# Performance work log

Hardware: AMD Instinct MI355X
Metric: run time of the kernel (lower is better)

## Reference

```python
import jax, jax.numpy as jnp
import numpy as np

# dims
D_IN, D, H, HD = 1536, 256, 8, 32
DEPTH, FFN = 2, 1024
B, L = 1, 8191
NGRIDS, TILE = 256, 256
SEGMENTS = [1024, 2048, 4096, 8192, 16384]   # get_optimal_segment_length(32768, 256)
RATIOS = [1, 2, 4, 8, 16]                    # LongNet canonical dilation ratios
SCALE = HD ** -0.5


def setup_inputs() -> dict:
    key = jax.random.key(0)
    ks = jax.random.split(key, 16)
    w = lambda k, s: jax.random.normal(k, s, jnp.float32) * 0.02
    return {
        "x": jax.random.normal(ks[0], (B, L, D_IN), jnp.float32),
        "coords": jax.random.randint(ks[1], (B, L, 2), 0, NGRIDS * TILE, jnp.int32),
        "proj_w": w(ks[2], (D_IN, D)), "proj_b": jnp.zeros((D,), jnp.float32),
        "cls_tok": w(ks[3], (1, 1, D)),
        "Wq": w(ks[4], (DEPTH, D, D)), "Wk": w(ks[5], (DEPTH, D, D)),
        "Wv": w(ks[6], (DEPTH, D, D)), "Wo": w(ks[7], (DEPTH, D, D)),
        "bq": jnp.zeros((DEPTH, D), jnp.float32), "bk": jnp.zeros((DEPTH, D), jnp.float32),
        "bv": jnp.zeros((DEPTH, D), jnp.float32), "bo": jnp.zeros((DEPTH, D), jnp.float32),
        "ln1_g": jnp.ones((DEPTH, D), jnp.float32), "ln1_b": jnp.zeros((DEPTH, D), jnp.float32),
        "ln2_g": jnp.ones((DEPTH, D), jnp.float32), "ln2_b": jnp.zeros((DEPTH, D), jnp.float32),
        "W1": w(ks[8], (DEPTH, D, FFN)), "b1": jnp.zeros((DEPTH, FFN), jnp.float32),
        "W2": w(ks[9], (DEPTH, FFN, D)), "b2": jnp.zeros((DEPTH, D), jnp.float32),
        "enc_g": jnp.ones((D,), jnp.float32), "enc_b": jnp.zeros((D,), jnp.float32),
        "norm_g": jnp.ones((D,), jnp.float32), "norm_b": jnp.zeros((D,), jnp.float32),
    }


def _ln(x, g, b):
    mu = x.mean(-1, keepdims=True)
    v = ((x - mu) ** 2).mean(-1, keepdims=True)
    return (x - mu) * jax.lax.rsqrt(v + 1e-5) * g + b


def _pos_table():
    # MAE-style 2D sincos pos embed, row 0 = cls (zeros). [NGRIDS^2+1, D]
    g = jnp.arange(NGRIDS, dtype=jnp.float32)
    gw, gh = jnp.meshgrid(g, g)  # gw[i,j]=j, gh[i,j]=i; flatten index = i*NGRIDS + j
    def one(pos):
        omega = 1.0 / (10000.0 ** (jnp.arange(D // 4, dtype=jnp.float32) / (D // 4)))
        o = pos.reshape(-1)[:, None] * omega[None]
        return jnp.concatenate([jnp.sin(o), jnp.cos(o)], -1)
    tab = jnp.concatenate([one(gw), one(gh)], -1)
    return jnp.concatenate([jnp.zeros((1, D), jnp.float32), tab], 0)


def _dilated_attn(q, k, v):
    # q,k,v: [B,S,H,HD]. LongNet: per (segment w, dilation r) branch, sparse in-segment
    # attention on stride-r rows (head-dependent offset h%r), branches fused via their
    # softmax log-sum-exp weights.
    S = q.shape[1]
    hh = jnp.arange(H)[:, None]
    outs, lses = [], []
    for w, r in zip(SEGMENTS, RATIOS):
        n = (S + w - 1) // w
        Sp = n * w
        def seg(t):
            tp = jnp.pad(t, ((0, 0), (0, Sp - S), (0, 0), (0, 0)))
            return tp.reshape(B, n, w, H, HD).transpose(0, 1, 3, 2, 4)  # [B,n,H,w,HD]
        qs_, ks_, vs_ = seg(q), seg(k), seg(v)
        t = w // r
        idx = (hh % r) + r * jnp.arange(t)[None, :]                  # [H,t]
        qs = qs_[:, :, hh, idx]                                      # [B,n,H,t,HD]
        ks = ks_[:, :, hh, idx]
        vs = vs_[:, :, hh, idx]
        valid = (jnp.arange(n)[:, None, None] * w + idx[None]) < S   # [n,H,t]
        sc = jnp.einsum('bnhtd,bnhsd->bnhts', qs, ks) * SCALE
        sc = jnp.where(valid[None, :, :, None, :], sc, -1e9)
        m = sc.max(-1, keepdims=True)
        p = jnp.exp(sc - m)
        den = p.sum(-1, keepdims=True)
        o = jnp.einsum('bnhts,bnhsd->bnhtd', p, vs) / den
        lse = m[..., 0] + jnp.log(den[..., 0])                       # [B,n,H,t]
        fo = jnp.zeros((B, n, H, w, HD), q.dtype).at[:, :, hh, idx].set(o)
        fl = jnp.full((B, n, H, w), -1e30, q.dtype).at[:, :, hh, idx].set(lse)
        outs.append(fo.transpose(0, 1, 3, 2, 4).reshape(B, Sp, H, HD)[:, :S])
        lses.append(fl.transpose(0, 1, 3, 2).reshape(B, Sp, H)[:, :S])
    Ls = jnp.stack(lses)   # [5,B,S,H]
    Os = jnp.stack(outs)   # [5,B,S,H,HD]
    wts = jnp.exp(Ls - Ls.max(0, keepdims=True))
    return (wts[..., None] * Os).sum(0) / wts.sum(0)[..., None]


def _forward(x, coords, proj_w, proj_b, cls_tok, Wq, Wk, Wv, Wo, bq, bk, bv, bo,
             ln1_g, ln1_b, ln2_g, ln2_b, W1, b1, W2, b2, enc_g, enc_b, norm_g, norm_b):
    h = x @ proj_w + proj_b                                   # patch embed [B,L,D]
    tab = _pos_table()
    cg = jnp.floor(coords.astype(jnp.float32) / TILE).astype(jnp.int32)
    pos = cg[..., 0] * NGRIDS + cg[..., 1] + 1                # coords_to_pos
    h = h + tab[pos]
    cls = jnp.broadcast_to(cls_tok + tab[0], (B, 1, D))
    h = jnp.concatenate([cls, h], 1)                          # [B,S,D], S = L+1
    S = h.shape[1]
    for i in range(DEPTH):                                    # pre-LN LongNet encoder layers
        a = _ln(h, ln1_g[i], ln1_b[i])
        q = (a @ Wq[i] + bq[i]).reshape(B, S, H, HD)
        k = (a @ Wk[i] + bk[i]).reshape(B, S, H, HD)
        v = (a @ Wv[i] + bv[i]).reshape(B, S, H, HD)
        o = _dilated_attn(q, k, v).reshape(B, S, D)
        h = h + o @ Wo[i] + bo[i]
        f = _ln(h, ln2_g[i], ln2_b[i])
        h = h + jax.nn.gelu(f @ W1[i] + b1[i], approximate=False) @ W2[i] + b2[i]
    h = _ln(h, enc_g, enc_b)     # encoder final LN
    h = _ln(h, norm_g, norm_b)   # model self.norm
    return h[:, 0]               # cls embedding (global_pool=False)


def reference(x, coords, proj_w, proj_b, cls_tok, Wq, Wk, Wv, Wo, bq, bk, bv, bo,
              ln1_g, ln1_b, ln2_g, ln2_b, W1, b1, W2, b2, enc_g, enc_b, norm_g, norm_b):
    return _forward(x, coords, proj_w, proj_b, cls_tok, Wq, Wk, Wv, Wo, bq, bk, bv, bo,
                    ln1_g, ln1_b, ln2_g, ln2_b, W1, b1, W2, b2, enc_g, enc_b, norm_g, norm_b)
```

## Files before the change

### kernel.cpp

```cpp
#include <hip/hip_runtime.h>
#include <math.h>

#define S_TOT 8192
#define DD 256
#define NHEAD 8
#define HDSZ 32
#define ATT_SCALE 0.17677669529663687f
#define ATT_SCALE_LOG2E 0.25506601f

typedef short short8 __attribute__((ext_vector_type(8)));
typedef float f32x4 __attribute__((ext_vector_type(4)));
typedef unsigned short ushort;

#define OFF_PROJ 0
#define OFF_WQ0  393216
#define OFF_WK0  458752
#define OFF_WV0  524288
#define OFF_WO0  589824
#define OFF_W10  655360
#define OFF_W20  917504
#define OFF_WK1  1179648
#define OFF_WV1  1245184
#define OFF_WQ1  1310720
#define OFF_WO1  1376256
#define OFF_W11  1441792
#define OFF_W21  1703936
#define WBUF_TOT 1966080

__device__ inline ushort f2bf(float f) {
    union { float f; unsigned u; } c; c.f = f;
    unsigned u = c.u;
    u += 0x7fffu + ((u >> 16) & 1u);
    return (ushort)(u >> 16);
}
__device__ inline float bf2f(ushort u) {
    union { unsigned u; float f; } c; c.u = ((unsigned)u) << 16;
    return c.f;
}
__device__ inline float gelu_exact(float v) {
    return 0.5f * v * (1.0f + erff(v * 0.7071067811865475f));
}
__device__ inline float block_sum256(float v, float* red) {
    #pragma unroll
    for (int off = 32; off > 0; off >>= 1) v += __shfl_down(v, off, 64);
    const int wid = threadIdx.x >> 6, lane = threadIdx.x & 63;
    if (lane == 0) red[wid] = v;
    __syncthreads();
    const float s = red[0] + red[1] + red[2] + red[3];
    __syncthreads();
    return s;
}

__global__ __launch_bounds__(256)
void setup_kernel(const float* __restrict__ x, const float* __restrict__ proj_w,
                  const float* __restrict__ Wq, const float* __restrict__ Wk,
                  const float* __restrict__ Wv, const float* __restrict__ Wo,
                  const float* __restrict__ W1, const float* __restrict__ W2,
                  const float* __restrict__ bq, const float* __restrict__ bk,
                  const float* __restrict__ bv, const float* __restrict__ cls_tok,
                  ushort* __restrict__ wbuf, float* __restrict__ bqkv0,
                  float* __restrict__ bkv1, ushort* __restrict__ xbf,
                  float* __restrict__ h)
{
    const int b = blockIdx.x;
    const int t = threadIdx.x;
    if (b >= 482) {
        if (b == 6626) { h[t] = cls_tok[t]; return; }
        const int i = (b - 482) * 256 + t;
        const int n8 = 8191 * 1536 / 8;
        if (i >= n8) return;
        const float4 a0 = *(const float4*)(x + (size_t)i * 8);
        const float4 a1 = *(const float4*)(x + (size_t)i * 8 + 4);
        ushort tmp[8] = { f2bf(a0.x), f2bf(a0.y), f2bf(a0.z), f2bf(a0.w),
                          f2bf(a1.x), f2bf(a1.y), f2bf(a1.z), f2bf(a1.w) };
        *(uint4*)(xbf + (size_t)i * 8) = *(const uint4*)tmp;
        return;
    }
    if (b >= 480) {
        if (b == 480) {
            for (int i = t; i < 768; i += 256)
                bqkv0[i] = (i < 256) ? bq[i] : ((i < 512) ? bk[i - 256] : bv[i - 512]);
        } else {
            for (int i = t; i < 512; i += 256)
                bkv1[i] = (i < 256) ? bk[256 + i] : bv[i];
        }
        return;
    }
    const float* src; ushort* dst; int R, C, t0;
    if (b < 96)       { src = proj_w;        dst = wbuf + OFF_PROJ; R = 1536; C = 256;  t0 = 0;   }
    else if (b < 112) { src = Wq;            dst = wbuf + OFF_WQ0;  R = 256;  C = 256;  t0 = 96;  }
    else if (b < 128) { src = Wk;            dst = wbuf + OFF_WK0;  R = 256;  C = 256;  t0 = 112; }
    else if (b < 144) { src = Wv;            dst = wbuf + OFF_WV0;  R = 256;  C = 256;  t0 = 128; }
    else if (b < 160) { src = Wo;            dst = wbuf + OFF_WO0;  R = 256;  C = 256;  t0 = 144; }
    else if (b < 224) { src = W1;            dst = wbuf + OFF_W10;  R = 256;  C = 1024; t0 = 160; }
    else if (b < 288) { src = W2;            dst = wbuf + OFF_W20;  R = 1024; C = 256;  t0 = 224; }
    else if (b < 304) { src = Wk + 65536;    dst = wbuf + OFF_WK1;  R = 256;  C = 256;  t0 = 288; }
    else if (b < 320) { src = Wv + 65536;    dst = wbuf + OFF_WV1;  R = 256;  C = 256;  t0 = 304; }
    else if (b < 336) { src = Wq + 65536;    dst = wbuf + OFF_WQ1;  R = 256;  C = 256;  t0 = 320; }
    else if (b < 352) { src = Wo + 65536;    dst = wbuf + OFF_WO1;  R = 256;  C = 256;  t0 = 336; }
    else if (b < 416) { src = W1 + 262144;   dst = wbuf + OFF_W11;  R = 256;  C = 1024; t0 = 352; }
    else              { src = W2 + 262144;   dst = wbuf + OFF_W21;  R = 1024; C = 256;  t0 = 416; }
    const int lt = b - t0;
    const int tC = C >> 6;
    const int tr = lt / tC, tc = lt % tC;
    __shared__ ushort tile[64][68];
    const int col = t & 63;
    const int r4  = t >> 6;
    #pragma unroll
    for (int i = 0; i < 16; ++i) {
        const int row = i * 4 + r4;
        tile[row][col] = f2bf(src[(size_t)(tr * 64 + row) * C + tc * 64 + col]);
    }
    __syncthreads();
    #pragma unroll
    for (int i = 0; i < 16; ++i) {
        const int n = i * 4 + r4;
        dst[(size_t)(tc * 64 + n) * R + tr * 64 + col] = tile[col][n];
    }
}

__global__ __launch_bounds__(256)
void ln_kernel(const float* __restrict__ in, const float* __restrict__ g,
               const float* __restrict__ b, ushort* __restrict__ outp)
{
    __shared__ float red[4];
    const int row = blockIdx.x;
    const int d = threadIdx.x;
    const float xv = in[(size_t)row * DD + d];
    const float mu = block_sum256(xv, red) * (1.0f / 256.0f);
    const float dv = xv - mu;
    const float var = block_sum256(dv * dv, red) * (1.0f / 256.0f);
    outp[(size_t)row * DD + d] = f2bf(dv * rsqrtf(var + 1e-5f) * g[d] + b[d]);
}

template <int BN>
__global__ __launch_bounds__(256)
void gemm4_kernel(const ushort* __restrict__ A, const ushort* __restrict__ Bt,
                  const float* __restrict__ bias, void* __restrict__ Cv,
                  int M, int N, int K, int flags, const int* __restrict__ coords)
{
    __shared__ ushort As[2][64][64];
    __shared__ ushort Bs[2][BN][64];
    constexpr int NT = BN / 32;
    const int nx  = N / BN;
    const int ny8 = gridDim.x / (8 * nx);
    const int b   = blockIdx.x;
    const int c8  = b & 7;
    const int j   = b >> 3;
    const int m0  = (c8 * ny8 + j / nx) * 64;
    const int n0  = (j % nx) * BN;

    const int tid  = threadIdx.x;
    const int wave = tid >> 6;
    const int lane = tid & 63;
    const int lrow = lane & 15;
    const int quad = lane >> 4;
    const int wr = (wave >> 1) * 32;
    const int wc = (wave & 1) * (BN / 2);

    float* Cf  = (float*)Cv;
    ushort* Cb = (ushort*)Cv;

    f32x4 acc[2][NT];
    #pragma unroll
    for (int mt = 0; mt < 2; ++mt)
        #pragma unroll
        for (int nt = 0; nt < NT; ++nt)
            acc[mt][nt] = (f32x4){0.f, 0.f, 0.f, 0.f};

    const int srow = tid >> 3;
    const int scol = (tid & 7) * 16;

    #define STAGE(BUF, KK)                                                        \
    do {                                                                          \
        _Pragma("unroll")                                                         \
        for (int c = 0; c < 2; ++c) {                                             \
            const int row = c * 32 + srow;                                        \
            const int sb  = scol ^ ((row & 7) << 4);                              \
            const ushort* srcp = A + (size_t)(m0 + row) * K + (KK) + (sb >> 1);   \
            __builtin_amdgcn_global_load_lds(                                     \
                (const __attribute__((address_space(1))) void*)srcp,              \
                (__attribute__((address_space(3))) void*)&As[BUF][c * 32 + wave * 8][0], \
                16, 0, 0);                                                        \
        }                                                                         \
        _Pragma("unroll")                                                         \
        for (int c = 0; c < BN / 32; ++c) {                                       \
            const int row = c * 32 + srow;                                        \
            const int sb  = scol ^ ((row & 7) << 4);                              \
            const ushort* srcp = Bt + (size_t)(n0 + row) * K + (KK) + (sb >> 1);  \
            __builtin_amdgcn_global_load_lds(                                     \
                (const __attribute__((address_space(1))) void*)srcp,              \
                (__attribute__((address_space(3))) void*)&Bs[BUF][c * 32 + wave * 8][0], \
                16, 0, 0);                                                        \
        }                                                                         \
    } while (0)

    int cur = 0;
    STAGE(0, 0);
    __syncthreads();
    for (int kk = 0; kk < K; kk += 64) {
        if (kk + 64 < K) STAGE(cur ^ 1, kk + 64);
        #pragma unroll
        for (int ks = 0; ks < 2; ++ks) {
            short8 af[2], bfr[NT];
            #pragma unroll
            for (int mt = 0; mt < 2; ++mt) {
                const int row = wr + mt * 16 + lrow;
                const int cb  = (ks * 64 + quad * 16) ^ ((row & 7) << 4);
                af[mt] = *(const short8*)((const char*)&As[cur][row][0] + cb);
            }
            #pragma unroll
            for (int nt = 0; nt < NT; ++nt) {
                const int row = wc + nt * 16 + lrow;
                const int cb  = (ks * 64 + quad * 16) ^ ((row & 7) << 4);
                bfr[nt] = *(const short8*)((const char*)&Bs[cur][row][0] + cb);
            }
            #pragma unroll
            for (int mt = 0; mt < 2; ++mt)
                #pragma unroll
                for (int nt = 0; nt < NT; ++nt)
                    acc[mt][nt] = __builtin_amdgcn_mfma_f32_16x16x32_bf16(
                                      af[mt], bfr[nt], acc[mt][nt], 0, 0, 0);
        }
        __syncthreads();
        cur ^= 1;
    }
    #undef STAGE

    #pragma unroll
    for (int mt = 0; mt < 2; ++mt) {
        #pragma unroll
        for (int rg = 0; rg < 4; ++rg) {
            const int r = m0 + wr + mt * 16 + quad * 4 + rg;
            if (r >= M) continue;
            #pragma unroll
            for (int nt = 0; nt < NT; ++nt) {
                const int c = n0 + wc + nt * 16 + lrow;
                float vv = acc[mt][nt][rg] + bias[c];
                if (flags & 8) {
                    const int cg = coords[2 * r + ((c < 128) ? 1 : 0)] >> 8;
                    const float omega = 1.0f / powf(10000.0f, (float)(c & 63) * (1.0f / 64.0f));
                    const float o = (float)cg * omega;
                    vv += ((c & 64) == 0) ? sinf(o) : cosf(o);
                }
                if (flags & 2) vv = gelu_exact(vv);
                if (flags & 4) {
                    Cb[(size_t)r * N + c] = f2bf(vv);
                } else {
                    if (flags & 1) vv += Cf[(size_t)r * N + c];
                    Cf[(size_t)r * N + c] = vv;
                }
            }
        }
    }
}

__global__ __launch_bounds__(256)
void attn_mfma_kernel(const ushort* __restrict__ q, const ushort* __restrict__ k,
                      const ushort* __restrict__ v, float* __restrict__ bo5,
                      float* __restrict__ lse5, int qs)
{
    __shared__ ushort Kb[64][40];
    __shared__ ushort Vt[32][72];
    __shared__ ushort Pb[4][16][72];

    const int unit = blockIdx.x;
    const int segu = unit >> 3;
    const int head = unit & 7;
    int b2, n;
    if (segu < 8)        { b2 = 0; n = segu; }
    else if (segu < 12)  { b2 = 1; n = segu - 8; }
    else if (segu < 14)  { b2 = 2; n = segu - 12; }
    else if (segu == 14) { b2 = 3; n = 0; }
    else                 { b2 = 4; n = 0; }
    const int w  = 1024 << b2;
    const int rr = 1 << b2;
    const int base = n * w + (head & (rr - 1));

    int kEnd = (S_TOT - base + rr - 1) >> b2;
    if (kEnd > 1024) kEnd = 1024;
    if (blockIdx.y * 128 >= kEnd) return;

    const int tid  = threadIdx.x;
    const int wave = tid >> 6;
    const int lane = tid & 63;
    const int lrow = lane & 15;
    const int quad = lane >> 4;

    short8 qf[2];
    #pragma unroll
    for (int m = 0; m < 2; ++m) {
        const int j  = blockIdx.y * 128 + wave * 32 + m * 16 + lrow;
        const int pq = base + rr * j;
        qf[m] = *(const short8*)(q + (size_t)pq * qs + head * HDSZ + quad * 8);
    }

    f32x4 acc[2][2];
    float lsum[2][4];
    #pragma unroll
    for (int m = 0; m < 2; ++m) {
        #pragma unroll
        for (int dt = 0; dt < 2; ++dt) acc[m][dt] = (f32x4){0.f, 0.f, 0.f, 0.f};
        #pragma unroll
        for (int rg = 0; rg < 4; ++rg) lsum[m][rg] = 0.f;
    }

    const int skr = tid >> 2;
    const int sdb = (tid & 3) * 8;

    for (int kc = 0; kc < kEnd; kc += 64) {
        {
            const size_t prow = (size_t)(base + rr * (kc + skr)) * qs + head * HDSZ + sdb;
            *(uint4*)&Kb[skr][sdb] = *(const uint4*)(k + prow);
            const uint4 vv = *(const uint4*)(v + prow);
            const ushort* vp = (const ushort*)&vv;
            #pragma unroll
            for (int i = 0; i < 8; ++i) Vt[sdb + i][skr] = vp[i];
        }
        __syncthreads();

        short8 kf[4], vf[2][2];
        #pragma unroll
        for (int t = 0; t < 4; ++t)
            kf[t] = *(const short8*)&Kb[t * 16 + lrow][quad * 8];
        #pragma unroll
        for (int g = 0; g < 2; ++g)
            #pragma unroll
            for (int dt = 0; dt < 2; ++dt)
                vf[g][dt] = *(const short8*)&Vt[dt * 16 + lrow][g * 32 + quad * 8];

        #pragma unroll
        for (int m = 0; m < 2; ++m) {
            f32x4 sc[4];
            #pragma unroll
            for (int t = 0; t < 4; ++t)
                sc[t] = __builtin_amdgcn_mfma_f32_16x16x32_bf16(
                            qf[m], kf[t], (f32x4){0.f,0.f,0.f,0.f}, 0, 0, 0);
            float p[4][4];
            #pragma unroll
            for (int t = 0; t < 4; ++t)
                #pragma unroll
                for (int rg = 0; rg < 4; ++rg)
                    p[t][rg] = exp2f(sc[t][rg] * ATT_SCALE_LOG2E);
            #pragma unroll
            for (int rg = 0; rg < 4; ++rg)
                lsum[m][rg] += (p[0][rg] + p[1][rg]) + (p[2][rg] + p[3][rg]);
            #pragma unroll
            for (int t = 0; t < 4; ++t)
                #pragma unroll
                for (int rg = 0; rg < 4; ++rg)
                    Pb[wave][quad * 4 + rg][t * 16 + lrow] = f2bf(p[t][rg]);
            __threadfence_block();
            short8 pa[2];
            #pragma unroll
            for (int g = 0; g < 2; ++g)
                pa[g] = *(const short8*)&Pb[wave][lrow][g * 32 + quad * 8];
            #pragma unroll
            for (int g = 0; g < 2; ++g)
                #pragma unroll
                for (int dt = 0; dt < 2; ++dt)
                    acc[m][dt] = __builtin_amdgcn_mfma_f32_16x16x32_bf16(
                                     pa[g], vf[g][dt], acc[m][dt], 0, 0, 0);
        }
        __syncthreads();
    }

    #pragma unroll
    for (int m = 0; m < 2; ++m) {
        #pragma unroll
        for (int rg = 0; rg < 4; ++rg) {
            float li = lsum[m][rg];
            #pragma unroll
            for (int off = 1; off < 16; off <<= 1)
                li += __shfl_xor(li, off, 16);
            const int j  = blockIdx.y * 128 + wave * 32 + m * 16 + quad * 4 + rg;
            const int pq = base + rr * j;
            const float inv = 1.0f / li;
            float* dst = bo5 + ((size_t)b2 * S_TOT + pq) * DD + head * HDSZ;
            dst[lrow]      = acc[m][0][rg] * inv;
            dst[16 + lrow] = acc[m][1][rg] * inv;
            if (lrow == 0)
                lse5[((size_t)b2 * S_TOT + pq) * NHEAD + head] = __logf(li);
        }
    }
}

__global__ __launch_bounds__(64)
void attn_row0_kernel(const float* __restrict__ q, const ushort* __restrict__ k,
                      const ushort* __restrict__ v, float* __restrict__ bo5,
                      float* __restrict__ lse5, int kvs)
{
    const int b2 = blockIdx.x >> 3;
    const int head = blockIdx.x & 7;
    const int r = 1 << b2;
    if (head & (r - 1)) return;
    const int tid = threadIdx.x;
    float qreg[32];
    #pragma unroll
    for (int d = 0; d < 32; d += 4) {
        const float4 t4 = *(const float4*)(q + head * HDSZ + d);
        qreg[d] = t4.x; qreg[d+1] = t4.y; qreg[d+2] = t4.z; qreg[d+3] = t4.w;
    }
    float m = -3.0e38f, l = 0.f, o[32];
    #pragma unroll
    for (int d = 0; d < 32; ++d) o[d] = 0.f;
    for (int j = tid; j < 1024; j += 64) {
        const int pk = r * j;
        float s;
        if (pk < S_TOT) {
            float s0 = 0.f;
            #pragma unroll
            for (int d = 0; d < 32; d += 8) {
                const uint4 raw = *(const uint4*)(k + (size_t)pk * kvs + head * HDSZ + d);
                const ushort* kp = (const ushort*)&raw;
                #pragma unroll
                for (int i = 0; i < 8; ++i) s0 += qreg[d + i] * bf2f(kp[i]);
            }
            s = s0 * ATT_SCALE;
        } else s = -1.0e9f;
        const float mn = fmaxf(m, s);
        const float c = __expf(m - mn);
        const float e = __expf(s - mn);
        l = l * c + e; m = mn;
        if (pk < S_TOT) {
            #pragma unroll
            for (int d = 0; d < 32; d += 8) {
                const uint4 raw = *(const uint4*)(v + (size_t)pk * kvs + head * HDSZ + d);
                const ushort* vp = (const ushort*)&raw;
                #pragma unroll
                for (int i = 0; i < 8; ++i) o[d + i] = o[d + i] * c + e * bf2f(vp[i]);
            }
        } else {
            #pragma unroll
            for (int d = 0; d < 32; ++d) o[d] *= c;
        }
    }
    __shared__ float ms[64], ls[64], os[64][32];
    ms[tid] = m; ls[tid] = l;
    #pragma unroll
    for (int d = 0; d < 32; ++d) os[tid][d] = o[d];
    __syncthreads();
    for (int st = 32; st >= 1; st >>= 1) {
        if (tid < st) {
            const float m2 = ms[tid + st], l2 = ls[tid + st];
            const float mn = fmaxf(ms[tid], m2);
            const float c1 = __expf(ms[tid] - mn);
            const float c2 = __expf(m2 - mn);
            ls[tid] = ls[tid] * c1 + l2 * c2;
            ms[tid] = mn;
            for (int d = 0; d < 32; ++d) os[tid][d] = os[tid][d]*c1 + os[tid+st][d]*c2;
        }
        __syncthreads();
    }
    if (tid < 32) bo5[(size_t)b2 * S_TOT * DD + head * HDSZ + tid] = os[0][tid] / ls[0];
    if (tid == 0) lse5[(size_t)b2 * S_TOT * NHEAD + head] = ms[0] + __logf(ls[0]);
}

__global__ __launch_bounds__(256)
void combine_kernel(const float* __restrict__ bo5, const float* __restrict__ lse5,
                    ushort* __restrict__ attn)
{
    const int p = blockIdx.x;
    const int d = threadIdx.x;
    const int h = d >> 5;
    float lse[5];
    bool sel[5];
    float mx = -3.0e38f;
    #pragma unroll
    for (int b2 = 0; b2 < 5; ++b2) {
        const int r = 1 << b2;
        sel[b2] = ((p & (r - 1)) == (h & (r - 1)));
        if (sel[b2]) {
            lse[b2] = lse5[((size_t)b2 * S_TOT + p) * NHEAD + h];
            mx = fmaxf(mx, lse[b2]);
        }
    }
    float wsum = 0.f, acc = 0.f;
    #pragma unroll
    for (int b2 = 0; b2 < 5; ++b2) {
        if (sel[b2]) {
            const float wgt = __expf(lse[b2] - mx);
            wsum += wgt;
            acc += wgt * bo5[((size_t)b2 * S_TOT + p) * DD + d];
        }
    }
    attn[(size_t)p * DD + d] = f2bf(acc / wsum);
}

__global__ __launch_bounds__(256)
void tail_qrow_kernel(const float* __restrict__ h, const float* __restrict__ g,
                      const float* __restrict__ b, const ushort* __restrict__ Wt,
                      const float* __restrict__ bias, float* __restrict__ qrow0)
{
    __shared__ float red[4];
    __shared__ float as[256];
    const int d = threadIdx.x;
    const float xv = h[d];
    const float mu = block_sum256(xv, red) * (1.0f / 256.0f);
    const float dv = xv - mu;
    const float var = block_sum256(dv * dv, red) * (1.0f / 256.0f);
    as[d] = dv * rsqrtf(var + 1e-5f) * g[d] + b[d];
    __syncthreads();
    float acc = 0.f;
    for (int k2 = 0; k2 < 256; k2 += 8) {
        const short8 w8 = *(const short8*)&Wt[(size_t)d * 256 + k2];
        #pragma unroll
        for (int j = 0; j < 8; ++j) acc += as[k2 + j] * bf2f((ushort)w8[j]);
    }
    qrow0[d] = acc + bias[d];
}

__global__ __launch_bounds__(256)
void tail_mid_kernel(const float* __restrict__ bo5, const float* __restrict__ lse5,
                     float* __restrict__ h, const ushort* __restrict__ Wo1t,
                     const float* __restrict__ bo1, const float* __restrict__ g2,
                     const float* __restrict__ b2, float* __restrict__ f)
{
    __shared__ float red[4];
    __shared__ float att[256];
    const int d = threadIdx.x;
    const int hh = d >> 5;
    float lse[5]; bool sel[5]; float mx = -3.0e38f;
    #pragma unroll
    for (int bb = 0; bb < 5; ++bb) {
        const int r = 1 << bb;
        sel[bb] = ((hh & (r - 1)) == 0);
        if (sel[bb]) {
            lse[bb] = lse5[(size_t)bb * S_TOT * NHEAD + hh];
            mx = fmaxf(mx, lse[bb]);
        }
    }
    float wsum = 0.f, acc = 0.f;
    #pragma unroll
    for (int bb = 0; bb < 5; ++bb) {
        if (sel[bb]) {
            const float wgt = __expf(lse[bb] - mx);
            wsum += wgt;
            acc += wgt * bo5[(size_t)bb * S_TOT * DD + d];
        }
    }
    att[d] = acc / wsum;
    __syncthreads();
    float a2 = 0.f;
    for (int k2 = 0; k2 < 256; k2 += 8) {
        const short8 w8 = *(const short8*)&Wo1t[(size_t)d * 256 + k2];
        #pragma unroll
        for (int j = 0; j < 8; ++j) a2 += att[k2 + j] * bf2f((ushort)w8[j]);
    }
    const float hv = a2 + bo1[d] + h[d];
    h[d] = hv;
    const float mu = block_sum256(hv, red) * (1.0f / 256.0f);
    const float dv = hv - mu;
    const float var = block_sum256(dv * dv, red) * (1.0f / 256.0f);
    f[d] = dv * rsqrtf(var + 1e-5f) * g2[d] + b2[d];
}

__global__ __launch_bounds__(256)
void tail_ffn1_kernel(const float* __restrict__ f, const ushort* __restrict__ W11t,
                      const float* __restrict__ b11, float* __restrict__ midr0)
{
    __shared__ float fs[256];
    const int tid = threadIdx.x;
    fs[tid] = f[tid];
    __syncthreads();
    const int n = blockIdx.x * 256 + tid;
    float acc = 0.f;
    for (int k2 = 0; k2 < 256; k2 += 8) {
        const short8 w8 = *(const short8*)&W11t[(size_t)n * 256 + k2];
        #pragma unroll
        for (int j = 0; j < 8; ++j) acc += fs[k2 + j] * bf2f((ushort)w8[j]);
    }
    midr0[n] = gelu_exact(acc + b11[n]);
}

__global__ __launch_bounds__(256)
void tail_ffn2_kernel(const float* __restrict__ midr0, const ushort* __restrict__ W21t,
                      const float* __restrict__ b21, float* __restrict__ h)
{
    __shared__ float ms[1024];
    const int tid = threadIdx.x;
    for (int i = tid; i < 1024; i += 256) ms[i] = midr0[i];
    __syncthreads();
    const int n  = blockIdx.x * 64 + (tid >> 2);
    const int kq = (tid & 3) * 256;
    float acc = 0.f;
    for (int k2 = 0; k2 < 256; k2 += 8) {
        const short8 w8 = *(const short8*)&W21t[(size_t)n * 1024 + kq + k2];
        #pragma unroll
        for (int j = 0; j < 8; ++j) acc += ms[kq + k2 + j] * bf2f((ushort)w8[j]);
    }
    acc += __shfl_xor(acc, 1);
    acc += __shfl_xor(acc, 2);
    if ((tid & 3) == 0) h[n] = h[n] + acc + b21[n];
}

__global__ __launch_bounds__(256)
void tail_final_kernel(const float* __restrict__ h, const float* __restrict__ eg,
                       const float* __restrict__ eb, const float* __restrict__ ng,
                       const float* __restrict__ nb, float* __restrict__ out)
{
    __shared__ float red[4];
    const int d = threadIdx.x;
    float xv = h[d];
    {
        const float mu = block_sum256(xv, red) * (1.0f / 256.0f);
        const float dv = xv - mu;
        const float var = block_sum256(dv * dv, red) * (1.0f / 256.0f);
        xv = dv * rsqrtf(var + 1e-5f) * eg[d] + eb[d];
    }
    {
        const float mu = block_sum256(xv, red) * (1.0f / 256.0f);
        const float dv = xv - mu;
        const float var = block_sum256(dv * dv, red) * (1.0f / 256.0f);
        out[d] = dv * rsqrtf(var + 1e-5f) * ng[d] + nb[d];
    }
}

extern "C" void kernel_launch(void* const* d_in, const int* in_sizes, int n_in,
                              void* d_out, int out_size, void* d_ws, size_t ws_size,
                              hipStream_t stream)
{
    const float* x      = (const float*)d_in[0];
    const int*   coords = (const int*)  d_in[1];
    const float* proj_w = (const float*)d_in[2];
    const float* proj_b = (const float*)d_in[3];
    const float* cls_tok= (const float*)d_in[4];
    const float* Wq     = (const float*)d_in[5];
    const float* Wk     = (const float*)d_in[6];
    const float* Wv     = (const float*)d_in[7];
    const float* Wo     = (const float*)d_in[8];
    const float* bq     = (const float*)d_in[9];
    const float* bk     = (const float*)d_in[10];
    const float* bv     = (const float*)d_in[11];
    const float* bo_    = (const float*)d_in[12];
    const float* ln1_g  = (const float*)d_in[13];
    const float* ln1_b  = (const float*)d_in[14];
    const float* ln2_g  = (const float*)d_in[15];
    const float* ln2_b  = (const float*)d_in[16];
    const float* W1     = (const float*)d_in[17];
    const float* b1     = (const float*)d_in[18];
    const float* W2     = (const float*)d_in[19];
    const float* b2v    = (const float*)d_in[20];
    const float* enc_g  = (const float*)d_in[21];
    const float* enc_b  = (const float*)d_in[22];
    const float* norm_g = (const float*)d_in[23];
    const float* norm_b = (const float*)d_in[24];
    float* out = (float*)d_out;

    const size_t SD = (size_t)S_TOT * DD;
    float* ws   = (float*)d_ws;
    float* h    = ws;
    float* big  = h + SD;
    float* bo5  = big;
    ushort* xbf   = (ushort*)big;
    ushort* midbf = (ushort*)big;
    float* lse5 = big + 5 * SD;
    ushort* a_bf    = (ushort*)(lse5 + 5 * S_TOT * NHEAD);
    ushort* qkv_bf  = a_bf + SD;
    ushort* attn_bf = qkv_bf + 3 * SD;
    ushort* wbuf    = attn_bf + SD;
    float* bqkv0  = (float*)(wbuf + WBUF_TOT);
    float* bkv1   = bqkv0 + 768;
    float* qrow0  = bkv1 + 512;
    float* f_r0   = qrow0 + 256;
    float* midr0  = f_r0 + 256;

    auto gemm64 = [&](const ushort* A, const ushort* Bt, const float* bias, void* C,
                      int M, int N, int K, int flags) {
        gemm4_kernel<64><<<128 * (N / 64), 256, 0, stream>>>(A, Bt, bias, C, M, N, K,
                                                             flags, coords);
    };
    auto gemm128 = [&](const ushort* A, const ushort* Bt, const float* bias, void* C,
                       int M, int N, int K, int flags) {
        gemm4_kernel<128><<<128 * (N / 128), 256, 0, stream>>>(A, Bt, bias, C, M, N, K,
                                                               flags, coords);
    };

    setup_kernel<<<6627, 256, 0, stream>>>(x, proj_w, Wq, Wk, Wv, Wo, W1, W2,
                                           bq, bk, bv, cls_tok, wbuf, bqkv0, bkv1,
                                           xbf, h);

    gemm64(xbf, wbuf + OFF_PROJ, proj_b, h + DD, 8191, 256, 1536, 8);

    ln_kernel<<<S_TOT, 256, 0, stream>>>(h, ln1_g, ln1_b, a_bf);
    gemm128(a_bf, wbuf + OFF_WQ0, bqkv0, qkv_bf, 8192, 768, 256, 4);
    attn_mfma_kernel<<<dim3(128, 8), 256, 0, stream>>>(qkv_bf, qkv_bf + 256,
                                                       qkv_bf + 512, bo5, lse5, 768);
    combine_kernel<<<S_TOT, 256, 0, stream>>>(bo5, lse5, attn_bf);
    gemm64(attn_bf, wbuf + OFF_WO0, bo_, h, 8192, 256, 256, 1);
    ln_kernel<<<S_TOT, 256, 0, stream>>>(h, ln2_g, ln2_b, a_bf);
    gemm128(a_bf, wbuf + OFF_W10, b1, midbf, 8192, 1024, 256, 4 | 2);
    gemm64(midbf, wbuf + OFF_W20, b2v, h, 8192, 256, 1024, 1);

    ln_kernel<<<S_TOT, 256, 0, stream>>>(h, ln1_g + 256, ln1_b + 256, a_bf);
    gemm128(a_bf, wbuf + OFF_WK1, bkv1, qkv_bf, 8192, 512, 256, 4);
    tail_qrow_kernel<<<1, 256, 0, stream>>>(h, ln1_g + 256, ln1_b + 256,
                                            wbuf + OFF_WQ1, bq + 256, qrow0);
    attn_row0_kernel<<<40, 64, 0, stream>>>(qrow0, qkv_bf, qkv_bf + 256, bo5, lse5, 512);
    tail_mid_kernel<<<1, 256, 0, stream>>>(bo5, lse5, h, wbuf + OFF_WO1, bo_ + 256,
                                           ln2_g + 256, ln2_b + 256, f_r0);
    tail_ffn1_kernel<<<4, 256, 0, stream>>>(f_r0, wbuf + OFF_W11, b1 + 1024, midr0);
    tail_ffn2_kernel<<<4, 256, 0, stream>>>(midr0, wbuf + OFF_W21, b2v + 256, h);
    tail_final_kernel<<<1, 256, 0, stream>>>(h, enc_g, enc_b, norm_g, norm_b, out);
}
```

Before: 430.8 us.

## Prefetch K/V into registers, swizzle V transpose in LDS, fold softmax scale into Q

The attention kernel now loads the next 64-row K/V chunk into registers while the current chunk is being computed, which overlaps global-memory latency with the MFMA work. The transposed V tile in shared memory uses an XOR-style column swizzle so the scattered transposing stores and the later vector reads hit fewer bank conflicts. The softmax scale times log2(e) is moved into the epilogue of the QKV GEMM for the Q columns, removing a multiply per score from the inner loop. P is converted to bf16 with the packed v_cvt_pk_bf16_f32 instruction. Scaling Q before bf16 rounding shifts the numerics slightly, and the register prefetch raises register pressure.

```diff
diff --git a/kernel.cpp b/kernel.cpp
--- a/kernel.cpp
+++ b/kernel.cpp
@@ -39,6 +39,11 @@
 }
 __device__ inline float gelu_exact(float v) {
     return 0.5f * v * (1.0f + erff(v * 0.7071067811865475f));
+}
+__device__ inline unsigned cvtpk_bf16(float a, float b) {
+    unsigned r;
+    asm("v_cvt_pk_bf16_f32 %0, %1, %2" : "=v"(r) : "v"(a), "v"(b));
+    return r;
 }
 __device__ inline float block_sum256(float v, float* red) {
     #pragma unroll
@@ -243,6 +248,7 @@
                     const float o = (float)cg * omega;
                     vv += ((c & 64) == 0) ? sinf(o) : cosf(o);
                 }
+                if (flags & 16) { if (c < 256) vv *= ATT_SCALE_LOG2E; }
                 if (flags & 2) vv = gelu_exact(vv);
                 if (flags & 4) {
                     Cb[(size_t)r * N + c] = f2bf(vv);
@@ -307,17 +313,27 @@
 
     const int skr = tid >> 2;
     const int sdb = (tid & 3) * 8;
+    const int grp = tid & 3;
+    const int wcol = (2 * skr + 32 * grp) & 127;
+
+    size_t prow = (size_t)(base + rr * skr) * qs + head * HDSZ + sdb;
+    uint4 kreg = *(const uint4*)(k + prow);
+    uint4 vreg = *(const uint4*)(v + prow);
 
     for (int kc = 0; kc < kEnd; kc += 64) {
+        *(uint4*)&Kb[skr][sdb] = kreg;
         {
-            const size_t prow = (size_t)(base + rr * (kc + skr)) * qs + head * HDSZ + sdb;
-            *(uint4*)&Kb[skr][sdb] = *(const uint4*)(k + prow);
-            const uint4 vv = *(const uint4*)(v + prow);
-            const ushort* vp = (const ushort*)&vv;
-            #pragma unroll
-            for (int i = 0; i < 8; ++i) Vt[sdb + i][skr] = vp[i];
+            const ushort* vp = (const ushort*)&vreg;
+            #pragma unroll
+            for (int i = 0; i < 8; ++i)
+                *(ushort*)((char*)&Vt[sdb + i][0] + wcol) = vp[i];
         }
         __syncthreads();
+        if (kc + 64 < kEnd) {
+            prow = (size_t)(base + rr * (kc + 64 + skr)) * qs + head * HDSZ + sdb;
+            kreg = *(const uint4*)(k + prow);
+            vreg = *(const uint4*)(v + prow);
+        }
 
         short8 kf[4], vf[2][2];
         #pragma unroll
@@ -326,8 +342,11 @@
         #pragma unroll
         for (int g = 0; g < 2; ++g)
             #pragma unroll
-            for (int dt = 0; dt < 2; ++dt)
-                vf[g][dt] = *(const short8*)&Vt[dt * 16 + lrow][g * 32 + quad * 8];
+            for (int dt = 0; dt < 2; ++dt) {
+                const int row  = dt * 16 + lrow;
+                const int rcol = (g * 64 + quad * 16 + 32 * ((row >> 3) & 3)) & 127;
+                vf[g][dt] = *(const short8*)((const char*)&Vt[row][0] + rcol);
+            }
 
         #pragma unroll
         for (int m = 0; m < 2; ++m) {
@@ -341,15 +360,19 @@
             for (int t = 0; t < 4; ++t)
                 #pragma unroll
                 for (int rg = 0; rg < 4; ++rg)
-                    p[t][rg] = exp2f(sc[t][rg] * ATT_SCALE_LOG2E);
+                    p[t][rg] = exp2f(sc[t][rg]);
             #pragma unroll
             for (int rg = 0; rg < 4; ++rg)
                 lsum[m][rg] += (p[0][rg] + p[1][rg]) + (p[2][rg] + p[3][rg]);
             #pragma unroll
-            for (int t = 0; t < 4; ++t)
-                #pragma unroll
-                for (int rg = 0; rg < 4; ++rg)
-                    Pb[wave][quad * 4 + rg][t * 16 + lrow] = f2bf(p[t][rg]);
+            for (int t = 0; t < 4; ++t) {
+                const unsigned pw01 = cvtpk_bf16(p[t][0], p[t][1]);
+                const unsigned pw23 = cvtpk_bf16(p[t][2], p[t][3]);
+                Pb[wave][quad * 4 + 0][t * 16 + lrow] = (ushort)pw01;
+                Pb[wave][quad * 4 + 1][t * 16 + lrow] = (ushort)(pw01 >> 16);
+                Pb[wave][quad * 4 + 2][t * 16 + lrow] = (ushort)pw23;
+                Pb[wave][quad * 4 + 3][t * 16 + lrow] = (ushort)(pw23 >> 16);
+            }
             __threadfence_block();
             short8 pa[2];
             #pragma unroll
@@ -683,7 +706,7 @@
     gemm64(xbf, wbuf + OFF_PROJ, proj_b, h + DD, 8191, 256, 1536, 8);
 
     ln_kernel<<<S_TOT, 256, 0, stream>>>(h, ln1_g, ln1_b, a_bf);
-    gemm128(a_bf, wbuf + OFF_WQ0, bqkv0, qkv_bf, 8192, 768, 256, 4);
+    gemm128(a_bf, wbuf + OFF_WQ0, bqkv0, qkv_bf, 8192, 768, 256, 4 | 16);
     attn_mfma_kernel<<<dim3(128, 8), 256, 0, stream>>>(qkv_bf, qkv_bf + 256,
                                                        qkv_bf + 512, bo5, lse5, 768);
     combine_kernel<<<S_TOT, 256, 0, stream>>>(bo5, lse5, attn_bf);
```

After: 431.6 us. No clear change (+0.2%).
